# Performance work log

Measured on AMD Instinct MI355X. Metric: run time of the kernel, lower is better.

Reference implementation:

```python
import jax, jax.numpy as jnp
import numpy as np

EPS_LN = 1e-6


def _ln(x):
    m = jnp.mean(x, axis=-1, keepdims=True)
    v = jnp.mean((x - m) ** 2, axis=-1, keepdims=True)
    return (x - m) * jax.lax.rsqrt(v + EPS_LN)


def _rope(q, cos, sin):
    # q: [B,S,H,D]; cos/sin: [S, D//2]; rotate interleaved pairs
    q2 = q.reshape(q.shape[:-1] + (-1, 2))
    a, b = q2[..., 0], q2[..., 1]
    c = cos[None, :, None, :]
    s = sin[None, :, None, :]
    return jnp.stack([a * c - b * s, a * s + b * c], axis=-1).reshape(q.shape)


def _attn(q, k, v):
    # q:[B,Sq,H,D] k,v:[B,Sk,H,D] -> [B,Sq,H,D]; flash default scale 1/sqrt(D)
    D = q.shape[-1]
    scores = jnp.einsum('bqhd,bkhd->bhqk', q, k) / jnp.sqrt(jnp.asarray(D, q.dtype))
    p = jax.nn.softmax(scores, axis=-1)
    return jnp.einsum('bhqk,bkhd->bqhd', p, v)


def setup_inputs() -> dict:
    key = jax.random.key(0)
    C, H, S, T, B = 2048, 16, 1024, 256, 4
    Dh = C // H
    F = int(C * 4)
    L, Ly = B * S, B * T
    ks = jax.random.split(key, 24)

    def w(k, shape):
        return (jax.random.normal(k, shape, dtype=jnp.float32) * 0.02)

    # RoPE angle table: positions 0..S-1 with standard inverse frequencies
    inv_freq = 1.0 / (10000.0 ** (np.arange(0, Dh, 2, dtype=np.float32) / Dh))
    freqs = jnp.asarray(np.arange(S, dtype=np.float32)[:, None] * inv_freq[None, :])

    inp = {
        'x': jax.random.normal(ks[0], (L, C), dtype=jnp.float32),
        'y': jax.random.normal(ks[1], (Ly, C), dtype=jnp.float32),
        't': jax.random.normal(ks[2], (L, 6 * C), dtype=jnp.float32),
        'freqs': freqs,
        'scale_shift_table': jax.random.normal(ks[3], (6, C), dtype=jnp.float32) / (C ** 0.5),
        'Wq_s': w(ks[4], (C, C)), 'bq_s': jnp.zeros((C,), jnp.float32),
        'Wk_s': w(ks[5], (C, C)), 'bk_s': jnp.zeros((C,), jnp.float32),
        'Wv_s': w(ks[6], (C, C)), 'bv_s': jnp.zeros((C,), jnp.float32),
        'Wo_s': w(ks[7], (C, C)), 'bo_s': jnp.zeros((C,), jnp.float32),
        'Wq_c': w(ks[8], (C, C)), 'bq_c': jnp.zeros((C,), jnp.float32),
        'Wk_c': w(ks[9], (C, C)), 'bk_c': jnp.zeros((C,), jnp.float32),
        'Wv_c': w(ks[10], (C, C)), 'bv_c': jnp.zeros((C,), jnp.float32),
        'Wo_c': w(ks[11], (C, C)), 'bo_c': jnp.zeros((C,), jnp.float32),
        'W_fc1': w(ks[12], (F, C)), 'b_fc1': jnp.zeros((F,), jnp.float32),
        'W_fc2': w(ks[13], (C, F)), 'b_fc2': jnp.zeros((C,), jnp.float32),
        'seq_len': S,
        'txt_len': T,
    }
    return inp


def reference(x, y, t, freqs, scale_shift_table,
              Wq_s, bq_s, Wk_s, bk_s, Wv_s, bv_s, Wo_s, bo_s,
              Wq_c, bq_c, Wk_c, bk_c, Wv_c, bv_c, Wo_c, bo_c,
              W_fc1, b_fc1, W_fc2, b_fc2, seq_len, txt_len):
    L, C = x.shape
    Dh = 2 * freqs.shape[1]
    H = C // Dh
    B = L // seq_len
    cos, sin = jnp.cos(freqs), jnp.sin(freqs)

    # per-token AdaLN params (B here == total tokens in torch code)
    mods = scale_shift_table[None] + t.reshape(L, 6, C)
    shift_msa, scale_msa, gate_msa, shift_mlp, scale_mlp, gate_mlp = (
        mods[:, i, :] for i in range(6))

    # ---- self attention (AdaLN modulate + RoPE) ----
    xm = _ln(x) * (1.0 + scale_msa) + shift_msa
    q = (xm @ Wq_s.T + bq_s).reshape(B, seq_len, H, Dh)
    k = (xm @ Wk_s.T + bk_s).reshape(B, seq_len, H, Dh)
    v = (xm @ Wv_s.T + bv_s).reshape(B, seq_len, H, Dh)
    q = _rope(q, cos, sin)
    k = _rope(k, cos, sin)
    a = _attn(q, k, v).reshape(L, C)
    x = x + gate_msa * (a @ Wo_s.T + bo_s)

    # ---- cross attention (no norm/modulation/gate, no RoPE) ----
    q = (x @ Wq_c.T + bq_c).reshape(B, seq_len, H, Dh)
    k = (y @ Wk_c.T + bk_c).reshape(B, txt_len, H, Dh)
    v = (y @ Wv_c.T + bv_c).reshape(B, txt_len, H, Dh)
    a = _attn(q, k, v).reshape(L, C)
    x = x + (a @ Wo_c.T + bo_c)

    # ---- MLP with AdaLN modulate + gate ----
    xm = _ln(x) * (1.0 + scale_mlp) + shift_mlp
    h = jax.nn.gelu(xm @ W_fc1.T + b_fc1, approximate=True)
    x = x + gate_mlp * (h @ W_fc2.T + b_fc2)
    return x
```

## Files before the change

kernel.cpp:

```cpp
#include <hip/hip_runtime.h>
#include <stdint.h>

#define C_DIM 2048
#define H_NUM 16
#define DH    128
#define S_LEN 1024
#define T_LEN 256
#define B_SZ  4
#define L_ROWS 4096
#define LY_ROWS 1024
#define F_DIM 8192

typedef __attribute__((ext_vector_type(4))) float f32x4;
typedef __attribute__((ext_vector_type(8))) __bf16 bf16x8;
typedef __attribute__((ext_vector_type(4))) unsigned short us4;
typedef __attribute__((ext_vector_type(8))) unsigned short us8;
typedef unsigned short u16;

__device__ __forceinline__ u16 f2bf(float f) {
  union { float f; uint32_t u; } v; v.f = f;
  uint32_t r = v.u + 0x7FFFu + ((v.u >> 16) & 1u);
  return (u16)(r >> 16);
}
__device__ __forceinline__ float bf2f(u16 h) {
  union { uint32_t u; float f; } v; v.u = ((uint32_t)h) << 16;
  return v.f;
}

typedef __attribute__((address_space(1))) void gvoid;
typedef __attribute__((address_space(3))) void lvoid;
__device__ __forceinline__ void gl_lds16(const void* g, void* l) {
  __builtin_amdgcn_global_load_lds((gvoid*)g, (lvoid*)l, 16, 0, 0);
}

template<int N> __device__ __forceinline__ void wait_vmcnt() {
  if constexpr (N == 0) asm volatile("s_waitcnt vmcnt(0)" ::: "memory");
  else if constexpr (N == 4) asm volatile("s_waitcnt vmcnt(4)" ::: "memory");
  else if constexpr (N == 5) asm volatile("s_waitcnt vmcnt(5)" ::: "memory");
  else if constexpr (N == 6) asm volatile("s_waitcnt vmcnt(6)" ::: "memory");
}
__device__ __forceinline__ void barrier_raw() {
  asm volatile("s_barrier" ::: "memory");
}
__device__ __forceinline__ void lgkm0_pin() {
  asm volatile("s_waitcnt lgkmcnt(0)" ::: "memory");
  __builtin_amdgcn_sched_barrier(0);
}

__device__ __forceinline__ float gelu_fast(float val) {
  float z = 0.7978845608f * (val + 0.044715f * val * val * val);
  float e = __expf(2.f * z);
  float th = 1.f - 2.f / (e + 1.f);
  return 0.5f * val * (1.f + th);
}

__global__ void k_cvt(const float* __restrict__ src, u16* __restrict__ dst, int n) {
  int i = (blockIdx.x * blockDim.x + threadIdx.x) * 4;
  int stride = gridDim.x * blockDim.x * 4;
  for (; i < n; i += stride) {
    float4 v = *(const float4*)(src + i);
    us4 o;
    o[0] = f2bf(v.x); o[1] = f2bf(v.y); o[2] = f2bf(v.z); o[3] = f2bf(v.w);
    *(us4*)(dst + i) = o;
  }
}

template<int INBF>
__global__ __launch_bounds__(256)
void k_modln(const void* __restrict__ xin, const float* __restrict__ t,
             const float* __restrict__ tab, u16* __restrict__ out,
             int scale_idx, int shift_idx) {
  int row = blockIdx.x;
  int tid = threadIdx.x;
  int c0 = tid * 8;
  float v[8];
  if constexpr (INBF) {
    us8 a = *(const us8*)((const u16*)xin + (size_t)row * C_DIM + c0);
#pragma unroll
    for (int j = 0; j < 8; ++j) v[j] = bf2f(a[j]);
  } else {
    const float* xr = (const float*)xin + (size_t)row * C_DIM;
    float4 a = *(const float4*)(xr + c0);
    float4 b = *(const float4*)(xr + c0 + 4);
    v[0] = a.x; v[1] = a.y; v[2] = a.z; v[3] = a.w;
    v[4] = b.x; v[5] = b.y; v[6] = b.z; v[7] = b.w;
  }
  float s = 0.f, ss = 0.f;
#pragma unroll
  for (int j = 0; j < 8; ++j) { s += v[j]; ss += v[j] * v[j]; }
#pragma unroll
  for (int m = 1; m < 64; m <<= 1) { s += __shfl_xor(s, m); ss += __shfl_xor(ss, m); }
  __shared__ float red[8];
  int wid = tid >> 6;
  if ((tid & 63) == 0) { red[wid * 2] = s; red[wid * 2 + 1] = ss; }
  __syncthreads();
  s  = red[0] + red[2] + red[4] + red[6];
  ss = red[1] + red[3] + red[5] + red[7];
  float mean = s * (1.f / C_DIM);
  float var  = ss * (1.f / C_DIM) - mean * mean;
  float rstd = rsqrtf(var + 1e-6f);
  const float* trow = t + (size_t)row * (6 * C_DIM);
  const float* tsc = trow + scale_idx * C_DIM + c0;
  const float* tsh = trow + shift_idx * C_DIM + c0;
  const float* gsc = tab + scale_idx * C_DIM + c0;
  const float* gsh = tab + shift_idx * C_DIM + c0;
  us8 o;
#pragma unroll
  for (int j = 0; j < 8; ++j) {
    float scv = 1.f + gsc[j] + tsc[j];
    float shv = gsh[j] + tsh[j];
    o[j] = f2bf((v[j] - mean) * rstd * scv + shv);
  }
  *(us8*)(out + (size_t)row * C_DIM + c0) = o;
}

template<int EPI>
__global__ __launch_bounds__(512, 2)
void k_gemm5(const u16* __restrict__ A, const u16* __restrict__ W,
             const float* __restrict__ bias0, const float* __restrict__ bias1,
             const float* __restrict__ bias2,
             u16* __restrict__ o0, u16* __restrict__ o1, u16* __restrict__ o2,
             int sec_shift, int out_ld,
             int M, int N, int K, int lda, int ldw, int nbx) {
  __shared__ __align__(16) u16 lds[65536];

  int tid = threadIdx.x;
  int nwg = gridDim.x;
  int q8 = nwg >> 3, r8 = nwg & 7;
  int xcd = blockIdx.x & 7, local = blockIdx.x >> 3;
  int wgid = (xcd < r8 ? xcd * (q8 + 1) : r8 * (q8 + 1) + (xcd - r8) * q8) + local;
  int bx = wgid % nbx, by = wgid / nbx;
  int m0 = by * 256, n0 = bx * 256;

  int wid = tid >> 6, lane = tid & 63;
  int wm = wid >> 2, wn = wid & 3;
  int lr = lane & 15, lg = lane >> 4;
  int xorslot = lr & 7;
  int bcol = (wn & 1) * 64;

  int srow = tid >> 3;
  int scol = ((tid ^ (tid >> 3)) & 7) * 8;

  auto stA = [&](int buf, int h, int kt) {
    u16* dst = lds + (buf * 2 + h) * 8192 + tid * 8;
#pragma unroll
    for (int call = 0; call < 2; ++call) {
      int grow = m0 + h * 128 + call * 64 + srow;
      gl_lds16(A + (size_t)grow * lda + kt * 64 + scol, dst + call * 4096);
    }
  };
  auto stB = [&](int buf, int h, int kt) {
    u16* dst = lds + 32768 + (buf * 2 + h) * 8192 + tid * 8;
#pragma unroll
    for (int call = 0; call < 2; ++call) {
      int grow = n0 + h * 128 + call * 64 + srow;
      gl_lds16(W + (size_t)grow * ldw + kt * 64 + scol, dst + call * 4096);
    }
  };

  f32x4 zero4 = {0.f, 0.f, 0.f, 0.f};
  f32x4 acc[8][4];
#pragma unroll
  for (int m = 0; m < 8; ++m)
#pragma unroll
    for (int n = 0; n < 4; ++n) acc[m][n] = zero4;

  int NT = K >> 6, NJ = NT >> 1;
  stA(0, 0, 0); stA(0, 1, 0); stB(0, 0, 0); stB(0, 1, 0);
  stB(1, 0, 1); stA(1, 0, 1);
  wait_vmcnt<4>();
  barrier_raw();

  for (int j = 0; j < NJ; ++j) {
    bool nlast = (j + 1 < NJ);
    int t1 = 2 * j + 1, t2 = 2 * j + 2, t3 = 2 * j + 3;
#pragma unroll
    for (int buf = 0; buf < 2; ++buf) {
      const u16* Ah = lds + (buf * 2 + wm) * 8192;
      const u16* Bh = lds + 32768 + (buf * 2 + (wn >> 1)) * 8192;
      bf16x8 aR[4][2], b0[2][2], b1[2][2];

#pragma unroll
      for (int m = 0; m < 4; ++m) {
        int r = m * 16 + lr;
#pragma unroll
        for (int kk = 0; kk < 2; ++kk)
          aR[m][kk] = *(const bf16x8*)(Ah + r * 64 + (((kk << 2) | lg) ^ xorslot) * 8);
      }
#pragma unroll
      for (int n = 0; n < 2; ++n) {
        int r = bcol + n * 16 + lr;
#pragma unroll
        for (int kk = 0; kk < 2; ++kk)
          b0[n][kk] = *(const bf16x8*)(Bh + r * 64 + (((kk << 2) | lg) ^ xorslot) * 8);
      }
      if (buf == 0) stA(1, 1, t1);
      else if (nlast) stA(0, 1, t2);
      barrier_raw();
      lgkm0_pin();
      __builtin_amdgcn_s_setprio(1);
#pragma unroll
      for (int kk = 0; kk < 2; ++kk)
#pragma unroll
        for (int m = 0; m < 4; ++m)
#pragma unroll
          for (int n = 0; n < 2; ++n)
            acc[m][n] = __builtin_amdgcn_mfma_f32_16x16x32_bf16(aR[m][kk], b0[n][kk], acc[m][n], 0, 0, 0);
      __builtin_amdgcn_s_setprio(0);
      barrier_raw();

#pragma unroll
      for (int n = 0; n < 2; ++n) {
        int r = bcol + 32 + n * 16 + lr;
#pragma unroll
        for (int kk = 0; kk < 2; ++kk)
          b1[n][kk] = *(const bf16x8*)(Bh + r * 64 + (((kk << 2) | lg) ^ xorslot) * 8);
      }
      if (buf == 0) stB(1, 1, t1);
      else if (nlast) stB(0, 1, t2);
      barrier_raw();
      lgkm0_pin();
      __builtin_amdgcn_s_setprio(1);
#pragma unroll
      for (int kk = 0; kk < 2; ++kk)
#pragma unroll
        for (int m = 0; m < 4; ++m)
#pragma unroll
          for (int n = 0; n < 2; ++n)
            acc[m][2 + n] = __builtin_amdgcn_mfma_f32_16x16x32_bf16(aR[m][kk], b1[n][kk], acc[m][2 + n], 0, 0, 0);
      __builtin_amdgcn_s_setprio(0);
      barrier_raw();

#pragma unroll
      for (int m = 0; m < 4; ++m) {
        int r = 64 + m * 16 + lr;
#pragma unroll
        for (int kk = 0; kk < 2; ++kk)
          aR[m][kk] = *(const bf16x8*)(Ah + r * 64 + (((kk << 2) | lg) ^ xorslot) * 8);
      }
      if (nlast) { if (buf == 0) stB(0, 0, t2); else stB(1, 0, t3); }
      barrier_raw();
      lgkm0_pin();
      __builtin_amdgcn_s_setprio(1);
#pragma unroll
      for (int kk = 0; kk < 2; ++kk)
#pragma unroll
        for (int m = 0; m < 4; ++m)
#pragma unroll
          for (int n = 0; n < 2; ++n)
            acc[4 + m][2 + n] = __builtin_amdgcn_mfma_f32_16x16x32_bf16(aR[m][kk], b1[n][kk], acc[4 + m][2 + n], 0, 0, 0);
      __builtin_amdgcn_s_setprio(0);
      barrier_raw();

      if (nlast) { if (buf == 0) stA(0, 0, t2); else stA(1, 0, t3); }
      barrier_raw();
      __builtin_amdgcn_s_setprio(1);
#pragma unroll
      for (int kk = 0; kk < 2; ++kk)
#pragma unroll
        for (int m = 0; m < 4; ++m)
#pragma unroll
          for (int n = 0; n < 2; ++n)
            acc[4 + m][n] = __builtin_amdgcn_mfma_f32_16x16x32_bf16(aR[m][kk], b0[n][kk], acc[4 + m][n], 0, 0, 0);
      __builtin_amdgcn_s_setprio(0);
      if (nlast) wait_vmcnt<4>(); else wait_vmcnt<0>();
      barrier_raw();
    }
  }

#pragma unroll
  for (int mf = 0; mf < 8; ++mf) {
    int row0 = m0 + wm * 128 + mf * 16 + lg * 4;
#pragma unroll
    for (int nf = 0; nf < 4; ++nf) {
      int col = n0 + wn * 64 + nf * 16 + lr;
      if constexpr (EPI == 0) {
        int sec = col >> sec_shift;
        const float* bp = sec == 0 ? bias0 : (sec == 1 ? bias1 : bias2);
        u16* op = sec == 0 ? o0 : (sec == 1 ? o1 : o2);
        int cs = col & ((1 << sec_shift) - 1);
        float bv = bp[cs];
#pragma unroll
        for (int r = 0; r < 4; ++r)
          op[(size_t)(row0 + r) * out_ld + cs] = f2bf(acc[mf][nf][r] + bv);
      } else {
        float bv = bias0[col];
#pragma unroll
        for (int r = 0; r < 4; ++r)
          o0[(size_t)(row0 + r) * out_ld + col] = f2bf(gelu_fast(acc[mf][nf][r] + bv));
      }
    }
  }
}

template<int BM, int EPI>
__global__ __launch_bounds__(512, 2)
void k_gemm3(const u16* __restrict__ A, const u16* __restrict__ W,
             const float* __restrict__ bias0, const float* __restrict__ bias1,
             const float* __restrict__ bias2,
             u16* __restrict__ o0, u16* __restrict__ o1, u16* __restrict__ o2,
             int sec_shift, int out_ld,
             float* __restrict__ outF, const float* __restrict__ resid,
             const float* __restrict__ gate_t, const float* __restrict__ gate_tab,
             int M, int N, int K, int lda, int ldw, int nbx) {
  constexpr int HTA = (BM / 2) * 64;
  constexpr int HTB = 128 * 64;
  constexpr int ACALLS = BM / 128;
  constexpr int QM = BM / 64;
  constexpr int MFR = BM / 32;
  constexpr int VMN = 4 + ACALLS;
  constexpr int BOFF = 4 * HTA;
  __shared__ __align__(16) u16 lds[BOFF + 4 * HTB];

  int tid = threadIdx.x;
  int nwg = gridDim.x;
  int q8 = nwg >> 3, r8 = nwg & 7;
  int xcd = blockIdx.x & 7, local = blockIdx.x >> 3;
  int wgid = (xcd < r8 ? xcd * (q8 + 1) : r8 * (q8 + 1) + (xcd - r8) * q8) + local;
  int bx = wgid % nbx, by = wgid / nbx;
  int m0 = by * BM, n0 = bx * 256;

  int wid = tid >> 6, lane = tid & 63;
  int wm = wid >> 2, wn = wid & 3;
  int lr = lane & 15, lg = lane >> 4;
  int xorslot = lr & 7;
  int bcol = (wn & 1) * 64;

  int srow = tid >> 3;
  int scol = ((tid ^ (tid >> 3)) & 7) * 8;

  auto stA = [&](int h, int kt2) {
    int pt = kt2 & 1;
    u16* dst = lds + (pt * 2 + h) * HTA + tid * 8;
#pragma unroll
    for (int call = 0; call < ACALLS; ++call) {
      int grow = m0 + h * (BM / 2) + call * 64 + srow;
      gl_lds16(A + (size_t)grow * lda + kt2 * 64 + scol, dst + call * 4096);
    }
  };
  auto stB = [&](int h, int kt2) {
    int pt = kt2 & 1;
    u16* dst = lds + BOFF + (pt * 2 + h) * HTB + tid * 8;
#pragma unroll
    for (int call = 0; call < 2; ++call) {
      int grow = n0 + h * 128 + call * 64 + srow;
      gl_lds16(W + (size_t)grow * ldw + kt2 * 64 + scol, dst + call * 4096);
    }
  };

  f32x4 zero4 = {0.f, 0.f, 0.f, 0.f};
  f32x4 acc[MFR][4];
#pragma unroll
  for (int m = 0; m < MFR; ++m)
#pragma unroll
    for (int n = 0; n < 4; ++n) acc[m][n] = zero4;

  int NT2 = K >> 6;
  stA(0, 0); stA(1, 0); stB(0, 0); stB(1, 0);
  stB(0, 1); stB(1, 1); stA(0, 1);
  wait_vmcnt<VMN>();
  barrier_raw();

  for (int kt = 0; kt < NT2; ++kt) {
    int p = kt & 1;
    const u16* Ah = lds + (p * 2 + wm) * HTA;
    const u16* Bh = lds + BOFF + (p * 2 + (wn >> 1)) * HTB;
    bf16x8 aR[QM][2], bR0[2][2], bR1[2][2];
    bool st1 = (kt + 1) < NT2, st2 = (kt + 2) < NT2;

#pragma unroll
    for (int m = 0; m < QM; ++m) {
      int r = m * 16 + lr;
#pragma unroll
      for (int kk = 0; kk < 2; ++kk)
        aR[m][kk] = *(const bf16x8*)(Ah + r * 64 + (((kk << 2) | lg) ^ xorslot) * 8);
    }
#pragma unroll
    for (int n = 0; n < 2; ++n) {
      int r = bcol + n * 16 + lr;
#pragma unroll
      for (int kk = 0; kk < 2; ++kk)
        bR0[n][kk] = *(const bf16x8*)(Bh + r * 64 + (((kk << 2) | lg) ^ xorslot) * 8);
    }
    if (st1) stA(1, kt + 1);
    lgkm0_pin();
    __builtin_amdgcn_s_setprio(1);
#pragma unroll
    for (int kk = 0; kk < 2; ++kk)
#pragma unroll
      for (int m = 0; m < QM; ++m)
#pragma unroll
        for (int n = 0; n < 2; ++n)
          acc[m][n] = __builtin_amdgcn_mfma_f32_16x16x32_bf16(aR[m][kk], bR0[n][kk], acc[m][n], 0, 0, 0);
    __builtin_amdgcn_s_setprio(0);
    barrier_raw();

#pragma unroll
    for (int n = 0; n < 2; ++n) {
      int r = bcol + 32 + n * 16 + lr;
#pragma unroll
      for (int kk = 0; kk < 2; ++kk)
        bR1[n][kk] = *(const bf16x8*)(Bh + r * 64 + (((kk << 2) | lg) ^ xorslot) * 8);
    }
    lgkm0_pin();
    __builtin_amdgcn_s_setprio(1);
#pragma unroll
    for (int kk = 0; kk < 2; ++kk)
#pragma unroll
      for (int m = 0; m < QM; ++m)
#pragma unroll
        for (int n = 0; n < 2; ++n)
          acc[m][2 + n] = __builtin_amdgcn_mfma_f32_16x16x32_bf16(aR[m][kk], bR1[n][kk], acc[m][2 + n], 0, 0, 0);
    __builtin_amdgcn_s_setprio(0);
    barrier_raw();

#pragma unroll
    for (int m = 0; m < QM; ++m) {
      int r = (BM / 4) + m * 16 + lr;
#pragma unroll
      for (int kk = 0; kk < 2; ++kk)
        aR[m][kk] = *(const bf16x8*)(Ah + r * 64 + (((kk << 2) | lg) ^ xorslot) * 8);
    }
    if (st2) { stB(0, kt + 2); stB(1, kt + 2); }
    lgkm0_pin();
    __builtin_amdgcn_s_setprio(1);
#pragma unroll
    for (int kk = 0; kk < 2; ++kk)
#pragma unroll
      for (int m = 0; m < QM; ++m)
#pragma unroll
        for (int n = 0; n < 2; ++n)
          acc[QM + m][2 + n] = __builtin_amdgcn_mfma_f32_16x16x32_bf16(aR[m][kk], bR1[n][kk], acc[QM + m][2 + n], 0, 0, 0);
    __builtin_amdgcn_s_setprio(0);
    barrier_raw();

    if (st2) stA(0, kt + 2);
    __builtin_amdgcn_s_setprio(1);
#pragma unroll
    for (int kk = 0; kk < 2; ++kk)
#pragma unroll
      for (int m = 0; m < QM; ++m)
#pragma unroll
        for (int n = 0; n < 2; ++n)
          acc[QM + m][n] = __builtin_amdgcn_mfma_f32_16x16x32_bf16(aR[m][kk], bR0[n][kk], acc[QM + m][n], 0, 0, 0);
    __builtin_amdgcn_s_setprio(0);
    if (st2) wait_vmcnt<VMN>(); else wait_vmcnt<0>();
    barrier_raw();
  }

#pragma unroll
  for (int mf = 0; mf < MFR; ++mf) {
    int row0 = m0 + wm * (BM / 2) + mf * 16 + lg * 4;
#pragma unroll
    for (int nf = 0; nf < 4; ++nf) {
      int col = n0 + wn * 64 + nf * 16 + lr;
      if constexpr (EPI == 0) {
        int sec = col >> sec_shift;
        const float* bp = sec == 0 ? bias0 : (sec == 1 ? bias1 : bias2);
        u16* op = sec == 0 ? o0 : (sec == 1 ? o1 : o2);
        int cs = col & ((1 << sec_shift) - 1);
        float bv = bp[cs];
#pragma unroll
        for (int r = 0; r < 4; ++r)
          op[(size_t)(row0 + r) * out_ld + cs] = f2bf(acc[mf][nf][r] + bv);
      } else if constexpr (EPI == 6) {
        float bv = bias0[col];
        float gt = gate_tab[col];
#pragma unroll
        for (int r = 0; r < 4; ++r) {
          int row = row0 + r;
          size_t idx = (size_t)row * N + col;
          float g = gt + gate_t[(size_t)row * (6 * C_DIM) + col];
          o0[idx] = f2bf(resid[idx] + g * (acc[mf][nf][r] + bv));
        }
      } else if constexpr (EPI == 7) {
        float bv = bias0[col];
#pragma unroll
        for (int r = 0; r < 4; ++r) {
          size_t idx = (size_t)(row0 + r) * N + col;
          o0[idx] = f2bf(bf2f(o0[idx]) + acc[mf][nf][r] + bv);
        }
      } else {
        float bv = bias0[col];
        float gt = gate_tab[col];
#pragma unroll
        for (int r = 0; r < 4; ++r) {
          int row = row0 + r;
          size_t idx = (size_t)row * N + col;
          float g = gt + gate_t[(size_t)row * (6 * C_DIM) + col];
          outF[idx] = bf2f(((const u16*)o1)[idx]) + g * (acc[mf][nf][r] + bv);
        }
      }
    }
  }
}

__global__ void k_rope(u16* __restrict__ q, u16* __restrict__ k,
                       const float* __restrict__ freqs) {
  int idx = blockIdx.x * blockDim.x + threadIdx.x;
  int total = L_ROWS * C_DIM / 8;
  for (; idx < total; idx += gridDim.x * blockDim.x) {
    int e = idx * 8;
    int row = e >> 11;
    int col = e & (C_DIM - 1);
    int s = row & (S_LEN - 1);
    int i0 = (col & (DH - 1)) >> 1;
    float4 fr = *(const float4*)(freqs + s * (DH / 2) + i0);
    float cs[4], sn[4];
    float fv[4] = {fr.x, fr.y, fr.z, fr.w};
#pragma unroll
    for (int j = 0; j < 4; ++j) __sincosf(fv[j], &sn[j], &cs[j]);
    us8 qa = *(us8*)(q + e);
    us8 ka = *(us8*)(k + e);
#pragma unroll
    for (int p = 0; p < 4; ++p) {
      float a = bf2f(qa[2 * p]), b = bf2f(qa[2 * p + 1]);
      qa[2 * p]     = f2bf(a * cs[p] - b * sn[p]);
      qa[2 * p + 1] = f2bf(a * sn[p] + b * cs[p]);
      float a2 = bf2f(ka[2 * p]), b2 = bf2f(ka[2 * p + 1]);
      ka[2 * p]     = f2bf(a2 * cs[p] - b2 * sn[p]);
      ka[2 * p + 1] = f2bf(a2 * sn[p] + b2 * cs[p]);
    }
    *(us8*)(q + e) = qa;
    *(us8*)(k + e) = ka;
  }
}

__global__ void k_transpose_v(const u16* __restrict__ v, u16* __restrict__ vt, int Lkv) {
  __shared__ u16 tile[32][33];
  int bh = blockIdx.x, b = bh >> 4, h = bh & 15;
  int k0 = blockIdx.y * 32, d0 = blockIdx.z * 32;
  int tx = threadIdx.x, ty = threadIdx.y;
  const u16* src = v + (size_t)(b * Lkv) * C_DIM + h * DH;
#pragma unroll
  for (int j = 0; j < 32; j += 8)
    tile[ty + j][tx] = src[(size_t)(k0 + ty + j) * C_DIM + d0 + tx];
  __syncthreads();
  u16* dst = vt + (size_t)bh * DH * Lkv;
#pragma unroll
  for (int j = 0; j < 32; j += 8)
    dst[(size_t)(d0 + ty + j) * Lkv + k0 + tx] = tile[tx][ty + j];
}

__global__ __launch_bounds__(256)
void k_flash(const u16* __restrict__ Q, const u16* __restrict__ K,
             const u16* __restrict__ Vt, u16* __restrict__ O,
             int Lq, int Lkv, float scale) {
  __shared__ __align__(16) u16 lK[64 * 128];
  __shared__ __align__(16) u16 lV[128 * 64];
  __shared__ __align__(16) u16 lP[4][16 * 72];
  int bh = blockIdx.x, b = bh >> 4, h = bh & 15;
  int tid = threadIdx.x, wid = tid >> 6, lane = tid & 63;
  int lr = lane & 15, lg = lane >> 4;
  int q0 = blockIdx.y * 64 + wid * 16;
  const u16* Qb = Q + ((size_t)(b * Lq) + q0) * C_DIM + h * DH;
  const u16* Kb = K + (size_t)(b * Lkv) * C_DIM + h * DH;
  const u16* Vb = Vt + (size_t)bh * DH * Lkv;

  bf16x8 qf[4];
#pragma unroll
  for (int ks = 0; ks < 4; ++ks)
    qf[ks] = *(const bf16x8*)(Qb + (size_t)lr * C_DIM + ks * 32 + lg * 8);

  f32x4 zero4 = {0.f, 0.f, 0.f, 0.f};
  f32x4 o[8];
#pragma unroll
  for (int n = 0; n < 8; ++n) o[n] = zero4;
  float mrow[4] = {-3.0e38f, -3.0e38f, -3.0e38f, -3.0e38f};
  float lrow[4] = {0.f, 0.f, 0.f, 0.f};

  int nsteps = Lkv >> 6;
  for (int kt = 0; kt < nsteps; ++kt) {
#pragma unroll
    for (int i = 0; i < 4; ++i) {
      int flat = i * 4096 + tid * 16;
      int key = flat >> 8, inner = flat & 255;
      int ksrc = inner ^ ((key & 7) << 4);
      gl_lds16((const char*)Kb + ((size_t)(kt * 64 + key) * C_DIM) * 2 + ksrc, (char*)lK + flat);
      int d = flat >> 7, keyb = flat & 127;
      int vsrc = keyb ^ ((d & 7) << 4);
      gl_lds16((const char*)Vb + ((size_t)d * Lkv) * 2 + kt * 128 + vsrc, (char*)lV + flat);
    }
    __syncthreads();

    f32x4 sc[4];
#pragma unroll
    for (int c = 0; c < 4; ++c) sc[c] = zero4;
#pragma unroll
    for (int c = 0; c < 4; ++c) {
      int key = c * 16 + lr;
#pragma unroll
      for (int ks = 0; ks < 4; ++ks) {
        int off = (ks * 64 + lg * 16) ^ ((key & 7) << 4);
        bf16x8 kf = *(const bf16x8*)((const char*)lK + key * 256 + off);
        sc[c] = __builtin_amdgcn_mfma_f32_16x16x32_bf16(qf[ks], kf, sc[c], 0, 0, 0);
      }
    }
#pragma unroll
    for (int r = 0; r < 4; ++r) {
      float s0 = sc[0][r] * scale, s1 = sc[1][r] * scale;
      float s2 = sc[2][r] * scale, s3 = sc[3][r] * scale;
      float mx = fmaxf(fmaxf(s0, s1), fmaxf(s2, s3));
#pragma unroll
      for (int m = 1; m < 16; m <<= 1) mx = fmaxf(mx, __shfl_xor(mx, m));
      float mnew = fmaxf(mrow[r], mx);
      float alpha = exp2f((mrow[r] - mnew) * 1.44269504f);
      mrow[r] = mnew;
      float p0 = exp2f((s0 - mnew) * 1.44269504f);
      float p1 = exp2f((s1 - mnew) * 1.44269504f);
      float p2 = exp2f((s2 - mnew) * 1.44269504f);
      float p3 = exp2f((s3 - mnew) * 1.44269504f);
      float psum = p0 + p1 + p2 + p3;
#pragma unroll
      for (int m = 1; m < 16; m <<= 1) psum += __shfl_xor(psum, m);
      lrow[r] = lrow[r] * alpha + psum;
#pragma unroll
      for (int n = 0; n < 8; ++n) o[n][r] *= alpha;
      u16* pr = lP[wid] + (4 * lg + r) * 72;
      pr[lr]      = f2bf(p0);
      pr[16 + lr] = f2bf(p1);
      pr[32 + lr] = f2bf(p2);
      pr[48 + lr] = f2bf(p3);
    }
    asm volatile("s_waitcnt lgkmcnt(0)" ::: "memory");
    __builtin_amdgcn_sched_barrier(0);
#pragma unroll
    for (int half = 0; half < 2; ++half) {
      bf16x8 pf = *(const bf16x8*)(lP[wid] + lr * 72 + half * 32 + lg * 8);
#pragma unroll
      for (int n = 0; n < 8; ++n) {
        int d = n * 16 + lr;
        int off = (half * 64 + lg * 16) ^ ((d & 7) << 4);
        bf16x8 vf = *(const bf16x8*)((const char*)lV + d * 128 + off);
        o[n] = __builtin_amdgcn_mfma_f32_16x16x32_bf16(pf, vf, o[n], 0, 0, 0);
      }
    }
    __syncthreads();
  }

  u16* Ob = O + ((size_t)(b * Lq) + q0) * C_DIM + h * DH;
#pragma unroll
  for (int n = 0; n < 8; ++n) {
    int d = n * 16 + lr;
#pragma unroll
    for (int r = 0; r < 4; ++r) {
      int qr = 4 * lg + r;
      Ob[(size_t)qr * C_DIM + d] = f2bf(o[n][r] / lrow[r]);
    }
  }
}

extern "C" void kernel_launch(void* const* d_in, const int* in_sizes, int n_in,
                              void* d_out, int out_size, void* d_ws, size_t ws_size,
                              hipStream_t stream) {
  const float* x     = (const float*)d_in[0];
  const float* y     = (const float*)d_in[1];
  const float* t     = (const float*)d_in[2];
  const float* freqs = (const float*)d_in[3];
  const float* tab   = (const float*)d_in[4];
  const float* Wq_s = (const float*)d_in[5];
  const float* bq_s = (const float*)d_in[6];
  const float* Wk_s = (const float*)d_in[7];
  const float* bk_s = (const float*)d_in[8];
  const float* Wv_s = (const float*)d_in[9];
  const float* bv_s = (const float*)d_in[10];
  const float* Wo_s = (const float*)d_in[11];
  const float* bo_s = (const float*)d_in[12];
  const float* Wq_c = (const float*)d_in[13];
  const float* bq_c = (const float*)d_in[14];
  const float* Wk_c = (const float*)d_in[15];
  const float* bk_c = (const float*)d_in[16];
  const float* Wv_c = (const float*)d_in[17];
  const float* bv_c = (const float*)d_in[18];
  const float* Wo_c = (const float*)d_in[19];
  const float* bo_c = (const float*)d_in[20];
  const float* W_fc1 = (const float*)d_in[21];
  const float* b_fc1 = (const float*)d_in[22];
  const float* W_fc2 = (const float*)d_in[23];
  const float* b_fc2 = (const float*)d_in[24];

  const size_t SZ_CC  = (size_t)C_DIM * C_DIM * 2;
  const size_t SZ_FC  = (size_t)F_DIM * C_DIM * 2;
  const size_t SZ_LC  = (size_t)L_ROWS * C_DIM * 2;
  const size_t SZ_YC  = (size_t)LY_ROWS * C_DIM * 2;
  char* ws = (char*)d_ws;
  size_t off = 0;
  u16* wq_s = (u16*)(ws + off); off += SZ_CC;
  u16* wk_s = (u16*)(ws + off); off += SZ_CC;
  u16* wv_s = (u16*)(ws + off); off += SZ_CC;
  u16* wo_s = (u16*)(ws + off); off += SZ_CC;
  u16* wq_c = (u16*)(ws + off); off += SZ_CC;
  u16* wk_c = (u16*)(ws + off); off += SZ_CC;
  u16* wv_c = (u16*)(ws + off); off += SZ_CC;
  u16* wo_c = (u16*)(ws + off); off += SZ_CC;
  u16* wfc1 = (u16*)(ws + off); off += SZ_FC;
  u16* wfc2 = (u16*)(ws + off); off += SZ_FC;
  u16* ybf  = (u16*)(ws + off); off += SZ_YC;
  u16* xm   = (u16*)(ws + off); off += SZ_LC;
  u16* qb   = (u16*)(ws + off); off += SZ_LC;
  u16* kb   = (u16*)(ws + off); off += SZ_LC;
  u16* vb   = (u16*)(ws + off); off += SZ_LC;
  u16* ao   = (u16*)(ws + off); off += SZ_LC;
  u16* hbuf = qb;
  u16* x1bf = (u16*)(ws + off); off += SZ_LC;
  u16* kc   = (u16*)(ws + off); off += SZ_YC;
  u16* vc   = (u16*)(ws + off); off += SZ_YC;
  u16* vt   = (u16*)(ws + off); off += SZ_LC;
  u16* vtc  = (u16*)(ws + off); off += SZ_YC;
  if (ws_size < off) return;

  auto cvt = [&](const float* s, u16* d, int n) {
    int blocks = (n / 4 + 255) / 256; if (blocks > 4096) blocks = 4096;
    k_cvt<<<blocks, 256, 0, stream>>>(s, d, n);
  };
  cvt(Wq_s, wq_s, C_DIM * C_DIM);
  cvt(Wk_s, wk_s, C_DIM * C_DIM);
  cvt(Wv_s, wv_s, C_DIM * C_DIM);
  cvt(Wo_s, wo_s, C_DIM * C_DIM);
  cvt(Wq_c, wq_c, C_DIM * C_DIM);
  cvt(Wk_c, wk_c, C_DIM * C_DIM);
  cvt(Wv_c, wv_c, C_DIM * C_DIM);
  cvt(Wo_c, wo_c, C_DIM * C_DIM);
  cvt(W_fc1, wfc1, F_DIM * C_DIM);
  cvt(W_fc2, wfc2, F_DIM * C_DIM);
  cvt(y, ybf, LY_ROWS * C_DIM);

  const float ascale = 0.08838834764831845f;

  k_modln<0><<<L_ROWS, 256, 0, stream>>>(x, t, tab, xm, 1, 0);
  k_gemm5<0><<<16 * 24, 512, 0, stream>>>(
      xm, wq_s, bq_s, bk_s, bv_s, qb, kb, vb, 11, C_DIM,
      L_ROWS, 6144, C_DIM, C_DIM, C_DIM, 24);
  k_rope<<<2048, 256, 0, stream>>>(qb, kb, freqs);
  k_transpose_v<<<dim3(B_SZ * H_NUM, S_LEN / 32, DH / 32), dim3(32, 8), 0, stream>>>(vb, vt, S_LEN);
  k_flash<<<dim3(B_SZ * H_NUM, S_LEN / 64), 256, 0, stream>>>(qb, kb, vt, ao, S_LEN, S_LEN, ascale);
  k_gemm3<128, 6><<<32 * 8, 512, 0, stream>>>(
      ao, wo_s, bo_s, nullptr, nullptr, x1bf, nullptr, nullptr, 30, C_DIM,
      nullptr, x, t + 2 * C_DIM, tab + 2 * C_DIM, L_ROWS, C_DIM, C_DIM, C_DIM, C_DIM, 8);
  k_gemm3<128, 0><<<32 * 8, 512, 0, stream>>>(
      x1bf, wq_c, bq_c, nullptr, nullptr, qb, nullptr, nullptr, 30, C_DIM,
      nullptr, nullptr, nullptr, nullptr, L_ROWS, C_DIM, C_DIM, C_DIM, C_DIM, 8);
  k_gemm3<128, 0><<<8 * 16, 512, 0, stream>>>(
      ybf, wk_c, bk_c, bv_c, bv_c, kc, vc, vc, 11, C_DIM,
      nullptr, nullptr, nullptr, nullptr, LY_ROWS, 4096, C_DIM, C_DIM, C_DIM, 16);
  k_transpose_v<<<dim3(B_SZ * H_NUM, T_LEN / 32, DH / 32), dim3(32, 8), 0, stream>>>(vc, vtc, T_LEN);
  k_flash<<<dim3(B_SZ * H_NUM, S_LEN / 64), 256, 0, stream>>>(qb, kc, vtc, ao, S_LEN, T_LEN, ascale);
  k_gemm3<128, 7><<<32 * 8, 512, 0, stream>>>(
      ao, wo_c, bo_c, nullptr, nullptr, x1bf, nullptr, nullptr, 30, C_DIM,
      nullptr, nullptr, nullptr, nullptr, L_ROWS, C_DIM, C_DIM, C_DIM, C_DIM, 8);
  k_modln<1><<<L_ROWS, 256, 0, stream>>>(x1bf, t, tab, xm, 4, 3);
  k_gemm5<1><<<16 * 32, 512, 0, stream>>>(
      xm, wfc1, b_fc1, nullptr, nullptr, hbuf, nullptr, nullptr, 30, F_DIM,
      L_ROWS, F_DIM, C_DIM, C_DIM, C_DIM, 32);
  k_gemm3<128, 8><<<32 * 8, 512, 0, stream>>>(
      hbuf, wfc2, b_fc2, nullptr, nullptr, nullptr, x1bf, nullptr, 30, C_DIM,
      (float*)d_out, nullptr, t + 5 * C_DIM, tab + 5 * C_DIM, L_ROWS, C_DIM, F_DIM, F_DIM, F_DIM, 8);
}
```

Measured before the change: 856.5 us.

## Batch weight conversions, fold log2e into attention scale, use gemm3 for QKV

After: 843.0 us. About the same (-1.6%).

```diff
diff --git a/kernel.cpp b/kernel.cpp
--- a/kernel.cpp
+++ b/kernel.cpp
@@ -59,6 +59,46 @@
   int stride = gridDim.x * blockDim.x * 4;
   for (; i < n; i += stride) {
     float4 v = *(const float4*)(src + i);
+    us4 o;
+    o[0] = f2bf(v.x); o[1] = f2bf(v.y); o[2] = f2bf(v.z); o[3] = f2bf(v.w);
+    *(us4*)(dst + i) = o;
+  }
+}
+
+__global__ void k_cvt8(const float* __restrict__ s0, const float* __restrict__ s1,
+                       const float* __restrict__ s2, const float* __restrict__ s3,
+                       const float* __restrict__ s4, const float* __restrict__ s5,
+                       const float* __restrict__ s6, const float* __restrict__ s7,
+                       u16* __restrict__ dst) {
+  const int PER = C_DIM * C_DIM;
+  int i = (blockIdx.x * blockDim.x + threadIdx.x) * 4;
+  int stride = gridDim.x * blockDim.x * 4;
+  int total = PER * 8;
+  for (; i < total; i += stride) {
+    int t = i >> 22;
+    const float* s;
+    switch (t) {
+      case 0: s = s0; break; case 1: s = s1; break;
+      case 2: s = s2; break; case 3: s = s3; break;
+      case 4: s = s4; break; case 5: s = s5; break;
+      case 6: s = s6; break; default: s = s7; break;
+    }
+    float4 v = *(const float4*)(s + (i & (PER - 1)));
+    us4 o;
+    o[0] = f2bf(v.x); o[1] = f2bf(v.y); o[2] = f2bf(v.z); o[3] = f2bf(v.w);
+    *(us4*)(dst + i) = o;
+  }
+}
+
+__global__ void k_cvt2(const float* __restrict__ s0, const float* __restrict__ s1,
+                       u16* __restrict__ dst) {
+  const int PER = F_DIM * C_DIM;
+  int i = (blockIdx.x * blockDim.x + threadIdx.x) * 4;
+  int stride = gridDim.x * blockDim.x * 4;
+  int total = PER * 2;
+  for (; i < total; i += stride) {
+    const float* s = (i >> 24) ? s1 : s0;
+    float4 v = *(const float4*)(s + (i & (PER - 1)));
     us4 o;
     o[0] = f2bf(v.x); o[1] = f2bf(v.y); o[2] = f2bf(v.z); o[3] = f2bf(v.w);
     *(us4*)(dst + i) = o;
@@ -545,7 +585,7 @@
 __global__ __launch_bounds__(256)
 void k_flash(const u16* __restrict__ Q, const u16* __restrict__ K,
              const u16* __restrict__ Vt, u16* __restrict__ O,
-             int Lq, int Lkv, float scale) {
+             int Lq, int Lkv, float scale2) {
   __shared__ __align__(16) u16 lK[64 * 128];
   __shared__ __align__(16) u16 lV[128 * 64];
   __shared__ __align__(16) u16 lP[4][16 * 72];
@@ -598,18 +638,18 @@
     }
 #pragma unroll
     for (int r = 0; r < 4; ++r) {
-      float s0 = sc[0][r] * scale, s1 = sc[1][r] * scale;
-      float s2 = sc[2][r] * scale, s3 = sc[3][r] * scale;
+      float s0 = sc[0][r] * scale2, s1 = sc[1][r] * scale2;
+      float s2 = sc[2][r] * scale2, s3 = sc[3][r] * scale2;
       float mx = fmaxf(fmaxf(s0, s1), fmaxf(s2, s3));
 #pragma unroll
       for (int m = 1; m < 16; m <<= 1) mx = fmaxf(mx, __shfl_xor(mx, m));
       float mnew = fmaxf(mrow[r], mx);
-      float alpha = exp2f((mrow[r] - mnew) * 1.44269504f);
+      float alpha = exp2f(mrow[r] - mnew);
       mrow[r] = mnew;
-      float p0 = exp2f((s0 - mnew) * 1.44269504f);
-      float p1 = exp2f((s1 - mnew) * 1.44269504f);
-      float p2 = exp2f((s2 - mnew) * 1.44269504f);
-      float p3 = exp2f((s3 - mnew) * 1.44269504f);
+      float p0 = exp2f(s0 - mnew);
+      float p1 = exp2f(s1 - mnew);
+      float p2 = exp2f(s2 - mnew);
+      float p3 = exp2f(s3 - mnew);
       float psum = p0 + p1 + p2 + p3;
 #pragma unroll
       for (int m = 1; m < 16; m <<= 1) psum += __shfl_xor(psum, m);
@@ -709,31 +749,19 @@
   u16* vtc  = (u16*)(ws + off); off += SZ_YC;
   if (ws_size < off) return;
 
-  auto cvt = [&](const float* s, u16* d, int n) {
-    int blocks = (n / 4 + 255) / 256; if (blocks > 4096) blocks = 4096;
-    k_cvt<<<blocks, 256, 0, stream>>>(s, d, n);
-  };
-  cvt(Wq_s, wq_s, C_DIM * C_DIM);
-  cvt(Wk_s, wk_s, C_DIM * C_DIM);
-  cvt(Wv_s, wv_s, C_DIM * C_DIM);
-  cvt(Wo_s, wo_s, C_DIM * C_DIM);
-  cvt(Wq_c, wq_c, C_DIM * C_DIM);
-  cvt(Wk_c, wk_c, C_DIM * C_DIM);
-  cvt(Wv_c, wv_c, C_DIM * C_DIM);
-  cvt(Wo_c, wo_c, C_DIM * C_DIM);
-  cvt(W_fc1, wfc1, F_DIM * C_DIM);
-  cvt(W_fc2, wfc2, F_DIM * C_DIM);
-  cvt(y, ybf, LY_ROWS * C_DIM);
-
-  const float ascale = 0.08838834764831845f;
+  k_cvt8<<<4096, 256, 0, stream>>>(Wq_s, Wk_s, Wv_s, Wo_s, Wq_c, Wk_c, Wv_c, Wo_c, wq_s);
+  k_cvt2<<<4096, 256, 0, stream>>>(W_fc1, W_fc2, wfc1);
+  k_cvt<<<2048, 256, 0, stream>>>(y, ybf, LY_ROWS * C_DIM);
+
+  const float ascale2 = 0.08838834764831845f * 1.44269504f;
 
   k_modln<0><<<L_ROWS, 256, 0, stream>>>(x, t, tab, xm, 1, 0);
-  k_gemm5<0><<<16 * 24, 512, 0, stream>>>(
+  k_gemm3<128, 0><<<32 * 24, 512, 0, stream>>>(
       xm, wq_s, bq_s, bk_s, bv_s, qb, kb, vb, 11, C_DIM,
-      L_ROWS, 6144, C_DIM, C_DIM, C_DIM, 24);
+      nullptr, nullptr, nullptr, nullptr, L_ROWS, 6144, C_DIM, C_DIM, C_DIM, 24);
   k_rope<<<2048, 256, 0, stream>>>(qb, kb, freqs);
   k_transpose_v<<<dim3(B_SZ * H_NUM, S_LEN / 32, DH / 32), dim3(32, 8), 0, stream>>>(vb, vt, S_LEN);
-  k_flash<<<dim3(B_SZ * H_NUM, S_LEN / 64), 256, 0, stream>>>(qb, kb, vt, ao, S_LEN, S_LEN, ascale);
+  k_flash<<<dim3(B_SZ * H_NUM, S_LEN / 64), 256, 0, stream>>>(qb, kb, vt, ao, S_LEN, S_LEN, ascale2);
   k_gemm3<128, 6><<<32 * 8, 512, 0, stream>>>(
       ao, wo_s, bo_s, nullptr, nullptr, x1bf, nullptr, nullptr, 30, C_DIM,
       nullptr, x, t + 2 * C_DIM, tab + 2 * C_DIM, L_ROWS, C_DIM, C_DIM, C_DIM, C_DIM, 8);
@@ -744,7 +772,7 @@
       ybf, wk_c, bk_c, bv_c, bv_c, kc, vc, vc, 11, C_DIM,
       nullptr, nullptr, nullptr, nullptr, LY_ROWS, 4096, C_DIM, C_DIM, C_DIM, 16);
   k_transpose_v<<<dim3(B_SZ * H_NUM, T_LEN / 32, DH / 32), dim3(32, 8), 0, stream>>>(vc, vtc, T_LEN);
-  k_flash<<<dim3(B_SZ * H_NUM, S_LEN / 64), 256, 0, stream>>>(qb, kc, vtc, ao, S_LEN, T_LEN, ascale);
+  k_flash<<<dim3(B_SZ * H_NUM, S_LEN / 64), 256, 0, stream>>>(qb, kc, vtc, ao, S_LEN, T_LEN, ascale2);
   k_gemm3<128, 7><<<32 * 8, 512, 0, stream>>>(
       ao, wo_c, bo_c, nullptr, nullptr, x1bf, nullptr, nullptr, 30, C_DIM,
       nullptr, nullptr, nullptr, nullptr, L_ROWS, C_DIM, C_DIM, C_DIM, C_DIM, 8);
```
